# Performance work log

Measured on AMD Instinct MI355X. Metric: run time of the kernel, lower is better.

The kernel has to match this reference:

```python
import jax, jax.numpy as jnp
import numpy as np

B = 512        # batch
H = 512        # hidden_dim
IN = 128       # input_dim = output_dim(1) + y_dim(127)
YD = 127       # y feature dim
ZD = H - YD    # z1 dim = 385
L = 256        # sequence length


def setup_inputs() -> dict:
    key = jax.random.key(0)
    ks = jax.random.split(key, 14)
    s = 1.0 / np.sqrt(H)  # pytorch GRUCell/Linear init scale
    u = lambda k, shape: jax.random.uniform(k, shape, jnp.float32, -s, s)
    return {
        "z1": jax.random.normal(ks[0], (B, ZD), jnp.float32),
        "y": jax.random.normal(ks[1], (B, YD), jnp.float32),
        "x": jax.random.normal(ks[2], (B, 1), jnp.float32),
        "hidden_1": jax.random.normal(ks[3], (B, H), jnp.float32),
        # GRUCell 1 (input IN -> hidden H)
        "w_ih1": u(ks[4], (3 * H, IN)),
        "w_hh1": u(ks[5], (3 * H, H)),
        "b_ih1": u(ks[6], (3 * H,)),
        "b_hh1": u(ks[7], (3 * H,)),
        # GRUCell 2 (hidden H -> hidden H)
        "w_ih2": u(ks[8], (3 * H, H)),
        "w_hh2": u(ks[9], (3 * H, H)),
        "b_ih2": u(ks[10], (3 * H,)),
        "b_hh2": u(ks[11], (3 * H,)),
        # output Linear (H -> 1)
        "w_fc": u(ks[12], (1, H)),
        "b_fc": u(ks[13], (1,)),
        "seq_len": L,
    }


def gru_cell(x, h, w_ih, w_hh, b_ih, b_hh):
    # PyTorch GRUCell gate order: r, z, n
    gi = x @ w_ih.T + b_ih            # [B, 3H]
    gh = h @ w_hh.T + b_hh            # [B, 3H]
    i_r, i_z, i_n = jnp.split(gi, 3, axis=1)
    h_r, h_z, h_n = jnp.split(gh, 3, axis=1)
    r = jax.nn.sigmoid(i_r + h_r)
    z = jax.nn.sigmoid(i_z + h_z)
    n = jnp.tanh(i_n + r * h_n)
    return (1.0 - z) * n + z * h


def reference(z1, y, x, hidden_1, w_ih1, w_hh1, b_ih1, b_hh1,
              w_ih2, w_hh2, b_ih2, b_hh2, w_fc, b_fc, seq_len):
    s0 = jnp.concatenate([z1, y], axis=1)   # [B, H]
    s1 = hidden_1                            # [B, H]
    inp = jnp.concatenate([x, y], axis=1)    # [B, IN]

    def step(carry, _):
        inp, s0, s1 = carry
        s0 = gru_cell(inp, s0, w_ih1, w_hh1, b_ih1, b_hh1)
        s1 = gru_cell(s0, s1, w_ih2, w_hh2, b_ih2, b_hh2)
        out = jax.nn.relu(s1 @ w_fc.T + b_fc)          # [B, 1]
        inp = jnp.concatenate([out, y], axis=1)         # [B, IN]
        return (inp, s0, s1), out[:, 0]

    _, outs = jax.lax.scan(step, (inp, s0, s1), None, length=seq_len)
    return outs.T  # [B, seq_len] == torch.cat(GenerOut, dim=1)
```

## Files before the change

### kernel.cpp

```cpp
#include <hip/hip_runtime.h>
#include <hip/hip_cooperative_groups.h>
#include <math.h>

namespace cg = cooperative_groups;

#define NB   256
#define NT   256
#define BSZ  512
#define HSZ  512
#define LSEQ 256
#define G3H  1536

typedef __attribute__((ext_vector_type(8))) short sh8;
typedef __attribute__((ext_vector_type(4))) float f4;

#define MFMA(a,b,c) __builtin_amdgcn_mfma_f32_16x16x32_bf16((a),(b),(c),0,0,0)
#define AGENT __HIP_MEMORY_SCOPE_AGENT
#define WGRP  __HIP_MEMORY_SCOPE_WORKGROUP
#define RLX   __ATOMIC_RELAXED

__device__ __forceinline__ float bf2f(unsigned short u) {
    union { unsigned int i; float f; } v; v.i = ((unsigned int)u) << 16; return v.f;
}
__device__ __forceinline__ unsigned short f2bf(float f) {
    union { float f; unsigned int i; } v; v.f = f;
    unsigned int r = v.i + 0x7fffu + ((v.i >> 16) & 1u);
    return (unsigned short)(r >> 16);
}
__device__ __forceinline__ float sigm(float v) { return 1.f / (1.f + __expf(-v)); }
__device__ __forceinline__ float tanh_(float v) { return 1.f - 2.f / (1.f + __expf(2.f * v)); }

__device__ __forceinline__ int xcc_id() {
    int x;
    asm volatile("s_getreg_b32 %0, hwreg(HW_REG_XCC_ID)" : "=s"(x));
    return x & 7;
}

struct P {
    const float *z1, *y, *x, *h1;
    const float *w_ih1, *w_hh1, *b_ih1, *b_hh1;
    const float *w_ih2, *w_hh2, *b_ih2, *b_hh2;
    const float *w_fc, *b_fc;
    unsigned short *wb1, *wb2, *wbI;
    unsigned short *giy;
    unsigned short *s0h[2], *s0l[2];
    unsigned short *s1h[2], *s1l[2];
    float *accT;
    unsigned *bar;
    unsigned *claim;
    float *out;
};

__global__ __launch_bounds__(256) void init_k(P p)
{
    int gt = blockIdx.x * 256 + threadIdx.x;
    int stride = gridDim.x * 256;
    for (int i = gt; i < G3H * HSZ; i += stride) {
        p.wb1[i] = f2bf(p.w_hh1[i]);
        p.wb2[i] = f2bf(p.w_hh2[i]);
        p.wbI[i] = f2bf(p.w_ih2[i]);
    }
    for (int i = gt; i < BSZ * HSZ; i += stride) {
        int b = i >> 9, hh = i & 511;
        float v0 = (hh < 385) ? p.z1[b * 385 + hh] : p.y[b * 127 + (hh - 385)];
        unsigned short u = f2bf(v0);
        p.s0h[0][i] = u; p.s0l[0][i] = f2bf(v0 - bf2f(u));
        float v1 = p.h1[i];
        u = f2bf(v1);
        p.s1h[0][i] = u; p.s1l[0][i] = f2bf(v1 - bf2f(u));
    }
    for (int i = gt; i < LSEQ * BSZ; i += stride) p.accT[i] = 0.f;
    for (int i = gt; i < 8 * 512; i += stride) p.bar[i] = 0u;
    for (int i = gt; i < 8; i += stride) p.claim[i] = 0u;
    for (int i = gt; i < BSZ * G3H; i += stride) {
        int b = i / G3H, j = i - b * G3H;
        float a = p.b_ih1[j];
        const float* yr = p.y + b * 127;
        const float* wr = p.w_ih1 + j * 128 + 1;
        #pragma unroll 4
        for (int k = 0; k < 127; ++k) a += yr[k] * wr[k];
        p.giy[i] = f2bf(a);
    }
}

__device__ __forceinline__ bool scan8p(unsigned* l0, unsigned* l1, unsigned* l2, unsigned* l3,
                                       unsigned* l4, unsigned* l5, unsigned* l6, unsigned* l7,
                                       unsigned tgt)
{
    unsigned r0, r1, r2, r3, r4, r5, r6, r7;
    unsigned z = 0;
    asm volatile(
        "global_atomic_add %0, %8, %16, off sc0\n\t"
        "global_atomic_add %1, %9, %16, off sc0\n\t"
        "global_atomic_add %2, %10, %16, off sc0\n\t"
        "global_atomic_add %3, %11, %16, off sc0\n\t"
        "global_atomic_add %4, %12, %16, off sc0\n\t"
        "global_atomic_add %5, %13, %16, off sc0\n\t"
        "global_atomic_add %6, %14, %16, off sc0\n\t"
        "global_atomic_add %7, %15, %16, off sc0\n\t"
        "s_waitcnt vmcnt(0)"
        : "=&v"(r0), "=&v"(r1), "=&v"(r2), "=&v"(r3),
          "=&v"(r4), "=&v"(r5), "=&v"(r6), "=&v"(r7)
        : "v"(l0), "v"(l1), "v"(l2), "v"(l3),
          "v"(l4), "v"(l5), "v"(l6), "v"(l7), "v"(z)
        : "memory");
    return (r0 >= tgt) & (r1 >= tgt) & (r2 >= tgt) & (r3 >= tgt)
         & (r4 >= tgt) & (r5 >= tgt) & (r6 >= tgt) & (r7 >= tgt);
}

__device__ __forceinline__ void gbar(unsigned* gb, int hx, unsigned bno, bool fast)
{
    __syncthreads();
    if (threadIdx.x == 0) {
        if (fast) {
            __hip_atomic_fetch_add(gb + (hx & 7) * 32, 1u, RLX, WGRP);
            unsigned tgt = 4u * bno;
            long g = 0;
            while (!scan8p(gb, gb + 32, gb + 64, gb + 96,
                           gb + 128, gb + 160, gb + 192, gb + 224, tgt)) {
                __builtin_amdgcn_s_sleep(1);
                if (++g > (1L << 24)) break;
            }
        } else {
            __hip_atomic_fetch_add(gb, 1u, __ATOMIC_RELEASE, AGENT);
            while (__hip_atomic_load(gb, RLX, AGENT) < 32u * bno)
                __builtin_amdgcn_s_sleep(1);
            __builtin_amdgcn_fence(__ATOMIC_ACQUIRE, "agent");
        }
    }
    __syncthreads();
    if (fast) {
        asm volatile("buffer_inv sc0\n\ts_waitcnt vmcnt(0)" ::: "memory");
    }
}

__global__ __launch_bounds__(NT, 1) void rnn_kernel(P p)
{
    __shared__ __align__(16) unsigned short W[9][16][520];
    __shared__ int s_xcd, s_slot;

    cg::grid_group grid = cg::this_grid();
    const int tid  = threadIdx.x;
    const int bid  = blockIdx.x;

    if (tid == 0) {
        int x = xcc_id();
        s_xcd = x;
        s_slot = (int)__hip_atomic_fetch_add(&p.claim[x], 1u, RLX, AGENT);
    }
    grid.sync();

    bool fast = true;
    #pragma unroll
    for (int x = 0; x < 8; ++x)
        fast = fast && (__hip_atomic_load(&p.claim[x], RLX, AGENT) == 32u);

    const int by = fast ? s_xcd  : (bid >> 5);
    const int hx = fast ? s_slot : (bid & 31);

    const int lane = tid & 63, w = tid >> 6;
    const int m = lane & 15, quad = lane >> 4;
    const int h0 = hx * 16, b0 = by * 64 + w * 16;
    const int h  = h0 + m;
    const int bA = b0 + m;
    const int bD = b0 + quad * 4;
    unsigned* gb = p.bar + by * 512;

    for (int c = tid; c < 9 * 1024; c += NT) {
        int mat = c >> 10, rem = c & 1023;
        int lc = rem >> 6, ch = rem & 63;
        const unsigned short* base =
            (mat < 3) ? (p.wb1 + (size_t)(mat * HSZ + h0 + lc) * HSZ)
          : (mat < 6) ? (p.wbI + (size_t)((mat - 3) * HSZ + h0 + lc) * HSZ)
                      : (p.wb2 + (size_t)((mat - 6) * HSZ + h0 + lc) * HSZ);
        *(sh8*)&W[mat][lc][ch * 8] = *((const sh8*)base + ch);
    }
    __syncthreads();

    const float bfc = p.b_fc[0];
    const int hq0 = h, hq1 = HSZ + h, hq2 = 2 * HSZ + h;
    const float bh1v0 = p.b_hh1[hq0], bh1v1 = p.b_hh1[hq1], bh1v2 = p.b_hh1[hq2];
    const float bi2v0 = p.b_ih2[hq0], bi2v1 = p.b_ih2[hq1], bi2v2 = p.b_ih2[hq2];
    const float bh2v0 = p.b_hh2[hq0], bh2v1 = p.b_hh2[hq1], bh2v2 = p.b_hh2[hq2];
    const float w0c0 = p.w_ih1[(size_t)hq0 * 128];
    const float w0c1 = p.w_ih1[(size_t)hq1 * 128];
    const float w0c2 = p.w_ih1[(size_t)hq2 * 128];
    const float wfcv = p.w_fc[h];

    float gyv[4][3];
    #pragma unroll
    for (int r = 0; r < 4; ++r) {
        gyv[r][0] = bf2f(p.giy[(size_t)(bD + r) * G3H + hq0]);
        gyv[r][1] = bf2f(p.giy[(size_t)(bD + r) * G3H + hq1]);
        gyv[r][2] = bf2f(p.giy[(size_t)(bD + r) * G3H + hq2]);
    }

    unsigned bno = 0;

    #pragma clang loop unroll(disable)
    for (int t = 0; t < LSEQ; ++t) {
        const int pi = t & 1, po = pi ^ 1;

        {
            const unsigned short* sh_ = p.s0h[pi];
            const unsigned short* sl_ = p.s0l[pi];
            const sh8* Ah = (const sh8*)sh_ + (size_t)bA * 64;
            const sh8* Al = (const sh8*)sl_ + (size_t)bA * 64;
            sh8 ah[16], al[16];
            #pragma unroll
            for (int ks = 0; ks < 16; ++ks) { ah[ks] = Ah[ks * 4 + quad]; al[ks] = Al[ks * 4 + quad]; }
            f4 a0 = {0.f,0.f,0.f,0.f}, a1 = a0, a2 = a0;
            #pragma unroll
            for (int ks = 0; ks < 16; ++ks) {
                const int fo = (ks * 4 + quad) * 8;
                sh8 w_r = *(const sh8*)&W[0][m][fo];
                sh8 w_z = *(const sh8*)&W[1][m][fo];
                sh8 w_n = *(const sh8*)&W[2][m][fo];
                a0 = MFMA(ah[ks], w_r, a0); a0 = MFMA(al[ks], w_r, a0);
                a1 = MFMA(ah[ks], w_z, a1); a1 = MFMA(al[ks], w_z, a1);
                a2 = MFMA(ah[ks], w_n, a2); a2 = MFMA(al[ks], w_n, a2);
            }
            unsigned short* oh = p.s0h[po];
            unsigned short* ol = p.s0l[po];
            #pragma unroll
            for (int r = 0; r < 4; ++r) {
                int b = bD + r;
                float o;
                if (t == 0) o = p.x[b];
                else {
                    float av = fast ? p.accT[(t - 1) * BSZ + b]
                                    : __hip_atomic_load(&p.accT[(t - 1) * BSZ + b], RLX, AGENT);
                    o = fmaxf(av + bfc, 0.f);
                }
                float rr = sigm(gyv[r][0] + o * w0c0 + a0[r] + bh1v0);
                float zz = sigm(gyv[r][1] + o * w0c1 + a1[r] + bh1v1);
                float nn = tanh_(gyv[r][2] + o * w0c2 + rr * (a2[r] + bh1v2));
                size_t ix = (size_t)b * HSZ + h;
                float so = bf2f(sh_[ix]) + bf2f(sl_[ix]);
                float sn = (1.f - zz) * nn + zz * so;
                unsigned short u = f2bf(sn);
                oh[ix] = u; ol[ix] = f2bf(sn - bf2f(u));
            }
        }
        ++bno; gbar(gb, hx, bno, fast);

        {
            const unsigned short* sh_ = p.s1h[pi];
            const unsigned short* sl_ = p.s1l[pi];
            const sh8* Aih = (const sh8*)p.s0h[po] + (size_t)bA * 64;
            const sh8* Ail = (const sh8*)p.s0l[po] + (size_t)bA * 64;
            const sh8* Ahh = (const sh8*)sh_ + (size_t)bA * 64;
            const sh8* Ahl = (const sh8*)sl_ + (size_t)bA * 64;

            sh8 ih[16], il[16];
            #pragma unroll
            for (int ks = 0; ks < 16; ++ks) { ih[ks] = Aih[ks * 4 + quad]; il[ks] = Ail[ks * 4 + quad]; }
            f4 ci0 = {0.f,0.f,0.f,0.f}, ci1 = ci0, ci2 = ci0;
            #pragma unroll
            for (int ks = 0; ks < 16; ++ks) {
                const int fo = (ks * 4 + quad) * 8;
                sh8 wir = *(const sh8*)&W[3][m][fo];
                sh8 wiz = *(const sh8*)&W[4][m][fo];
                sh8 win = *(const sh8*)&W[5][m][fo];
                ci0 = MFMA(ih[ks], wir, ci0); ci0 = MFMA(il[ks], wir, ci0);
                ci1 = MFMA(ih[ks], wiz, ci1); ci1 = MFMA(il[ks], wiz, ci1);
                ci2 = MFMA(ih[ks], win, ci2); ci2 = MFMA(il[ks], win, ci2);
            }
            sh8 hh[16], hl[16];
            #pragma unroll
            for (int ks = 0; ks < 16; ++ks) { hh[ks] = Ahh[ks * 4 + quad]; hl[ks] = Ahl[ks * 4 + quad]; }
            f4 ch0 = {0.f,0.f,0.f,0.f}, ch1 = ch0, ch2 = ch0;
            #pragma unroll
            for (int ks = 0; ks < 16; ++ks) {
                const int fo = (ks * 4 + quad) * 8;
                sh8 whr = *(const sh8*)&W[6][m][fo];
                sh8 whz = *(const sh8*)&W[7][m][fo];
                sh8 whn = *(const sh8*)&W[8][m][fo];
                ch0 = MFMA(hh[ks], whr, ch0); ch0 = MFMA(hl[ks], whr, ch0);
                ch1 = MFMA(hh[ks], whz, ch1); ch1 = MFMA(hl[ks], whz, ch1);
                ch2 = MFMA(hh[ks], whn, ch2); ch2 = MFMA(hl[ks], whn, ch2);
            }
            unsigned short* oh = p.s1h[po];
            unsigned short* ol = p.s1l[po];
            #pragma unroll
            for (int r = 0; r < 4; ++r) {
                int b = bD + r;
                float rr = sigm(ci0[r] + bi2v0 + ch0[r] + bh2v0);
                float zz = sigm(ci1[r] + bi2v1 + ch1[r] + bh2v1);
                float nn = tanh_(ci2[r] + bi2v2 + rr * (ch2[r] + bh2v2));
                size_t ix = (size_t)b * HSZ + h;
                float so = bf2f(sh_[ix]) + bf2f(sl_[ix]);
                float sn = (1.f - zz) * nn + zz * so;
                unsigned short u = f2bf(sn);
                oh[ix] = u; ol[ix] = f2bf(sn - bf2f(u));
                float c = sn * wfcv;
                c += __shfl_xor(c, 1); c += __shfl_xor(c, 2);
                c += __shfl_xor(c, 4); c += __shfl_xor(c, 8);
                if (m == 0) {
                    if (fast) __hip_atomic_fetch_add(&p.accT[t * BSZ + b], c, RLX, WGRP);
                    else      atomicAdd(&p.accT[t * BSZ + b], c);
                }
            }
        }
        ++bno; gbar(gb, hx, bno, fast);
    }

    {
        const int r = hx;
        for (int e = tid; e < 512; e += NT) {
            int idx = r * 512 + e;
            int bl = idx >> 8, t = idx & 255;
            int b = by * 64 + bl;
            float av = fast ? p.accT[t * BSZ + b]
                            : __hip_atomic_load(&p.accT[t * BSZ + b], RLX, AGENT);
            p.out[(size_t)b * 256 + t] = fmaxf(av + bfc, 0.f);
        }
    }
}

extern "C" void kernel_launch(void* const* d_in, const int* in_sizes, int n_in,
                              void* d_out, int out_size, void* d_ws, size_t ws_size,
                              hipStream_t stream)
{
    (void)in_sizes; (void)n_in; (void)out_size; (void)ws_size;
    P p;
    p.z1    = (const float*)d_in[0];
    p.y     = (const float*)d_in[1];
    p.x     = (const float*)d_in[2];
    p.h1    = (const float*)d_in[3];
    p.w_ih1 = (const float*)d_in[4];
    p.w_hh1 = (const float*)d_in[5];
    p.b_ih1 = (const float*)d_in[6];
    p.b_hh1 = (const float*)d_in[7];
    p.w_ih2 = (const float*)d_in[8];
    p.w_hh2 = (const float*)d_in[9];
    p.b_ih2 = (const float*)d_in[10];
    p.b_hh2 = (const float*)d_in[11];
    p.w_fc  = (const float*)d_in[12];
    p.b_fc  = (const float*)d_in[13];

    unsigned short* ws = (unsigned short*)d_ws;
    size_t off = 0;
    p.wb1 = ws + off; off += (size_t)G3H * HSZ;
    p.wb2 = ws + off; off += (size_t)G3H * HSZ;
    p.wbI = ws + off; off += (size_t)G3H * HSZ;
    p.giy = ws + off; off += (size_t)BSZ * G3H;
    for (int i = 0; i < 2; ++i) { p.s0h[i] = ws + off; off += (size_t)BSZ * HSZ; }
    for (int i = 0; i < 2; ++i) { p.s0l[i] = ws + off; off += (size_t)BSZ * HSZ; }
    for (int i = 0; i < 2; ++i) { p.s1h[i] = ws + off; off += (size_t)BSZ * HSZ; }
    for (int i = 0; i < 2; ++i) { p.s1l[i] = ws + off; off += (size_t)BSZ * HSZ; }
    p.accT  = (float*)(ws + off);    off += (size_t)LSEQ * BSZ * 2;
    p.bar   = (unsigned*)(ws + off); off += 8 * 512 * 2;
    p.claim = (unsigned*)(ws + off);
    p.out   = (float*)d_out;

    init_k<<<dim3(1024), dim3(256), 0, stream>>>(p);

    void* args[] = { &p };
    hipLaunchCooperativeKernel((const void*)rnn_kernel, dim3(NB), dim3(NT), args, 0, stream);
}
```

Baseline: 4.695 ms.

## Split grid barrier to overlap hidden-state GEMM with barrier wait

After: 4.362 ms. 7.1% less time.

```diff
diff --git a/kernel.cpp b/kernel.cpp
--- a/kernel.cpp
+++ b/kernel.cpp
@@ -108,12 +108,17 @@
          & (r4 >= tgt) & (r5 >= tgt) & (r6 >= tgt) & (r7 >= tgt);
 }
 
-__device__ __forceinline__ void gbar(unsigned* gb, int hx, unsigned bno, bool fast)
-{
-    __syncthreads();
+__device__ __forceinline__ void gbar_arrive(unsigned* gb, int hx, bool fast)
+{
+    if (threadIdx.x == 0) {
+        if (fast) __hip_atomic_fetch_add(gb + (hx & 7) * 32, 1u, RLX, WGRP);
+        else      __hip_atomic_fetch_add(gb, 1u, __ATOMIC_RELEASE, AGENT);
+    }
+}
+__device__ __forceinline__ void gbar_wait(unsigned* gb, unsigned bno, bool fast)
+{
     if (threadIdx.x == 0) {
         if (fast) {
-            __hip_atomic_fetch_add(gb + (hx & 7) * 32, 1u, RLX, WGRP);
             unsigned tgt = 4u * bno;
             long g = 0;
             while (!scan8p(gb, gb + 32, gb + 64, gb + 96,
@@ -122,9 +127,11 @@
                 if (++g > (1L << 24)) break;
             }
         } else {
-            __hip_atomic_fetch_add(gb, 1u, __ATOMIC_RELEASE, AGENT);
-            while (__hip_atomic_load(gb, RLX, AGENT) < 32u * bno)
+            long g = 0;
+            while (__hip_atomic_load(gb, RLX, AGENT) < 32u * bno) {
                 __builtin_amdgcn_s_sleep(1);
+                if (++g > (1L << 27)) break;
+            }
             __builtin_amdgcn_fence(__ATOMIC_ACQUIRE, "agent");
         }
     }
@@ -132,6 +139,12 @@
     if (fast) {
         asm volatile("buffer_inv sc0\n\ts_waitcnt vmcnt(0)" ::: "memory");
     }
+}
+__device__ __forceinline__ void gbar(unsigned* gb, int hx, unsigned bno, bool fast)
+{
+    __syncthreads();
+    gbar_arrive(gb, hx, fast);
+    gbar_wait(gb, bno, fast);
 }
 
 __global__ __launch_bounds__(NT, 1) void rnn_kernel(P p)
@@ -242,15 +255,41 @@
                 oh[ix] = u; ol[ix] = f2bf(sn - bf2f(u));
             }
         }
-        ++bno; gbar(gb, hx, bno, fast);
-
+        ++bno;
+        __syncthreads();
+        gbar_arrive(gb, hx, fast);
+
+        f4 ch0 = {0.f,0.f,0.f,0.f}, ch1 = ch0, ch2 = ch0;
+        float so1[4];
         {
             const unsigned short* sh_ = p.s1h[pi];
             const unsigned short* sl_ = p.s1l[pi];
+            const sh8* Ahh = (const sh8*)sh_ + (size_t)bA * 64;
+            const sh8* Ahl = (const sh8*)sl_ + (size_t)bA * 64;
+            sh8 hh[16], hl[16];
+            #pragma unroll
+            for (int ks = 0; ks < 16; ++ks) { hh[ks] = Ahh[ks * 4 + quad]; hl[ks] = Ahl[ks * 4 + quad]; }
+            #pragma unroll
+            for (int r = 0; r < 4; ++r) {
+                size_t ix = (size_t)(bD + r) * HSZ + h;
+                so1[r] = bf2f(sh_[ix]) + bf2f(sl_[ix]);
+            }
+            #pragma unroll
+            for (int ks = 0; ks < 16; ++ks) {
+                const int fo = (ks * 4 + quad) * 8;
+                sh8 whr = *(const sh8*)&W[6][m][fo];
+                sh8 whz = *(const sh8*)&W[7][m][fo];
+                sh8 whn = *(const sh8*)&W[8][m][fo];
+                ch0 = MFMA(hh[ks], whr, ch0); ch0 = MFMA(hl[ks], whr, ch0);
+                ch1 = MFMA(hh[ks], whz, ch1); ch1 = MFMA(hl[ks], whz, ch1);
+                ch2 = MFMA(hh[ks], whn, ch2); ch2 = MFMA(hl[ks], whn, ch2);
+            }
+        }
+        gbar_wait(gb, bno, fast);
+
+        {
             const sh8* Aih = (const sh8*)p.s0h[po] + (size_t)bA * 64;
             const sh8* Ail = (const sh8*)p.s0l[po] + (size_t)bA * 64;
-            const sh8* Ahh = (const sh8*)sh_ + (size_t)bA * 64;
-            const sh8* Ahl = (const sh8*)sl_ + (size_t)bA * 64;
 
             sh8 ih[16], il[16];
             #pragma unroll
@@ -266,20 +305,6 @@
                 ci1 = MFMA(ih[ks], wiz, ci1); ci1 = MFMA(il[ks], wiz, ci1);
                 ci2 = MFMA(ih[ks], win, ci2); ci2 = MFMA(il[ks], win, ci2);
             }
-            sh8 hh[16], hl[16];
-            #pragma unroll
-            for (int ks = 0; ks < 16; ++ks) { hh[ks] = Ahh[ks * 4 + quad]; hl[ks] = Ahl[ks * 4 + quad]; }
-            f4 ch0 = {0.f,0.f,0.f,0.f}, ch1 = ch0, ch2 = ch0;
-            #pragma unroll
-            for (int ks = 0; ks < 16; ++ks) {
-                const int fo = (ks * 4 + quad) * 8;
-                sh8 whr = *(const sh8*)&W[6][m][fo];
-                sh8 whz = *(const sh8*)&W[7][m][fo];
-                sh8 whn = *(const sh8*)&W[8][m][fo];
-                ch0 = MFMA(hh[ks], whr, ch0); ch0 = MFMA(hl[ks], whr, ch0);
-                ch1 = MFMA(hh[ks], whz, ch1); ch1 = MFMA(hl[ks], whz, ch1);
-                ch2 = MFMA(hh[ks], whn, ch2); ch2 = MFMA(hl[ks], whn, ch2);
-            }
             unsigned short* oh = p.s1h[po];
             unsigned short* ol = p.s1l[po];
             #pragma unroll
@@ -289,8 +314,7 @@
                 float zz = sigm(ci1[r] + bi2v1 + ch1[r] + bh2v1);
                 float nn = tanh_(ci2[r] + bi2v2 + rr * (ch2[r] + bh2v2));
                 size_t ix = (size_t)b * HSZ + h;
-                float so = bf2f(sh_[ix]) + bf2f(sl_[ix]);
-                float sn = (1.f - zz) * nn + zz * so;
+                float sn = (1.f - zz) * nn + zz * so1[r];
                 unsigned short u = f2bf(sn);
                 oh[ix] = u; ol[ix] = f2bf(sn - bf2f(u));
                 float c = sn * wfcv;
```
